# Kernel optimization log

Hardware: AMD Instinct MI355X
Metric: run time of the kernel (lower is better)

Reference implementation:

```python
import jax, jax.numpy as jnp
import numpy as np

N_AGENTS = 50000  # number of batch elements (agents); fixed num_segments
N_NEIGHBORS = 1600000  # total ragged neighbors flattened (avg degree 32)
STATE_DIM = 64
PHI_HID = 64
PHI_OUT = 64
RHO_HID = 64
ACT_DIM = 2


def setup_inputs() -> dict:
    key = jax.random.key(0)
    ks = jax.random.split(key, 6)
    s = lambda fan_in: 1.0 / np.sqrt(fan_in)
    neighbors = jax.random.normal(ks[0], (N_NEIGHBORS, STATE_DIM), dtype=jnp.float32)
    phi_w1 = jax.random.normal(ks[1], (STATE_DIM, PHI_HID), dtype=jnp.float32) * s(STATE_DIM)
    phi_b1 = jnp.zeros((PHI_HID,), dtype=jnp.float32)
    phi_w2 = jax.random.normal(ks[2], (PHI_HID, PHI_OUT), dtype=jnp.float32) * s(PHI_HID)
    phi_b2 = jnp.zeros((PHI_OUT,), dtype=jnp.float32)
    rho_w1 = jax.random.normal(ks[3], (PHI_OUT, RHO_HID), dtype=jnp.float32) * s(PHI_OUT)
    rho_b1 = jnp.zeros((RHO_HID,), dtype=jnp.float32)
    rho_w2 = jax.random.normal(ks[4], (RHO_HID, ACT_DIM), dtype=jnp.float32) * s(RHO_HID)
    rho_b2 = jnp.zeros((ACT_DIM,), dtype=jnp.float32)
    segment_ids = jnp.sort(jax.random.randint(ks[5], (N_NEIGHBORS,), 0, N_AGENTS, dtype=jnp.int32))
    return {
        "neighbors": neighbors,
        "phi_w1": phi_w1, "phi_b1": phi_b1, "phi_w2": phi_w2, "phi_b2": phi_b2,
        "rho_w1": rho_w1, "rho_b1": rho_b1, "rho_w2": rho_w2, "rho_b2": rho_b2,
        "segment_ids": segment_ids,
    }


def reference(neighbors, phi_w1, phi_b1, phi_w2, phi_b2,
              rho_w1, rho_b1, rho_w2, rho_b2, segment_ids):
    # phi MLP applied to every neighbor feature (vectorized over the flat ragged axis)
    h = jax.nn.relu(neighbors @ phi_w1 + phi_b1)          # [N_NEIGHBORS, PHI_HID]
    h = h @ phi_w2 + phi_b2                               # [N_NEIGHBORS, PHI_OUT]
    # per-agent sum over variable-length neighbor sets (the Python double loop in torch)
    summ = jax.ops.segment_sum(h, segment_ids, num_segments=N_AGENTS)  # [N_AGENTS, PHI_OUT]
    # rho MLP on pooled features
    r = jax.nn.relu(summ @ rho_w1 + rho_b1)               # [N_AGENTS, RHO_HID]
    return r @ rho_w2 + rho_b2                            # [N_AGENTS, ACT_DIM]
```

## Files before the change

kernel.cpp:

```cpp
#include <hip/hip_runtime.h>
#include <hip/hip_bf16.h>

#define N_AGENTS 50000
#define N_NEI    1600000
#define ROWS     128
#define PHI_BLOCKS (N_NEI / ROWS)

typedef __bf16 bf16_t;
typedef __attribute__((ext_vector_type(8))) __bf16 bf16x8;
typedef __attribute__((ext_vector_type(4))) __bf16 bf16x4;
typedef __attribute__((ext_vector_type(4))) float  f32x4;

#define SA 72
#define SO 66

__global__ __launch_bounds__(256) void phi_kernel(
    const float* __restrict__ nb,
    const float* __restrict__ w1g, const float* __restrict__ b1g,
    const float* __restrict__ w2g, const float* __restrict__ b2g,
    const int* __restrict__ seg, float* __restrict__ summ)
{
  __shared__ __align__(16) union {
    struct {
      bf16_t A[ROWS * SA];
      bf16_t Wt[2][64 * SA];
    } s;
    float outb[ROWS * SO];
  } u;
  __shared__ float biasf[2][64];
  __shared__ int sid[ROWS + 4];

  const int tid  = threadIdx.x;
  const int w    = tid >> 6;
  const int lane = tid & 63;
  const int m16  = lane & 15;
  const int q    = lane >> 4;
  const int base_row = blockIdx.x * ROWS;

  if (tid < ROWS) sid[tid] = seg[base_row + tid];
  if (tid < 64) biasf[0][tid] = b1g[tid];
  else if (tid < 128) biasf[1][tid - 64] = b2g[tid - 64];

  for (int i = tid; i < 4096; i += 256) {
    int k = i >> 6, n = i & 63;
    u.s.Wt[0][n * SA + k] = (bf16_t)w1g[i];
    u.s.Wt[1][n * SA + k] = (bf16_t)w2g[i];
  }

  {
    const float4* np4 = (const float4*)(nb + (size_t)base_row * 64);
    #pragma unroll
    for (int it = 0; it < 8; ++it) {
      int j = tid + it * 256;
      float4 v = np4[j];
      int row = j >> 4, col = (j & 15) * 4;
      bf16x4 p = { (bf16_t)v.x, (bf16_t)v.y, (bf16_t)v.z, (bf16_t)v.w };
      *(bf16x4*)&u.s.A[row * SA + col] = p;
    }
  }
  __syncthreads();

  const int rb = w * 32;
  bf16x8 bfr[4][2], afr[2][2];
  f32x4  acc[2][4];

  #pragma unroll
  for (int tn = 0; tn < 4; ++tn)
    #pragma unroll
    for (int kb = 0; kb < 2; ++kb)
      bfr[tn][kb] = *(const bf16x8*)&u.s.Wt[0][(tn * 16 + m16) * SA + kb * 32 + q * 8];
  #pragma unroll
  for (int tm = 0; tm < 2; ++tm)
    #pragma unroll
    for (int kb = 0; kb < 2; ++kb)
      afr[tm][kb] = *(const bf16x8*)&u.s.A[(rb + tm * 16 + m16) * SA + kb * 32 + q * 8];
  #pragma unroll
  for (int tm = 0; tm < 2; ++tm)
    #pragma unroll
    for (int tn = 0; tn < 4; ++tn) {
      f32x4 a = {0.f, 0.f, 0.f, 0.f};
      a = __builtin_amdgcn_mfma_f32_16x16x32_bf16(afr[tm][0], bfr[tn][0], a, 0, 0, 0);
      a = __builtin_amdgcn_mfma_f32_16x16x32_bf16(afr[tm][1], bfr[tn][1], a, 0, 0, 0);
      acc[tm][tn] = a;
    }
  #pragma unroll
  for (int tm = 0; tm < 2; ++tm)
    #pragma unroll
    for (int tn = 0; tn < 4; ++tn) {
      float bv = biasf[0][tn * 16 + m16];
      #pragma unroll
      for (int i = 0; i < 4; ++i) {
        float hv = fmaxf(acc[tm][tn][i] + bv, 0.f);
        u.s.A[(rb + tm * 16 + q * 4 + i) * SA + tn * 16 + m16] = (bf16_t)hv;
      }
    }

  #pragma unroll
  for (int tn = 0; tn < 4; ++tn)
    #pragma unroll
    for (int kb = 0; kb < 2; ++kb)
      bfr[tn][kb] = *(const bf16x8*)&u.s.Wt[1][(tn * 16 + m16) * SA + kb * 32 + q * 8];
  #pragma unroll
  for (int tm = 0; tm < 2; ++tm)
    #pragma unroll
    for (int kb = 0; kb < 2; ++kb)
      afr[tm][kb] = *(const bf16x8*)&u.s.A[(rb + tm * 16 + m16) * SA + kb * 32 + q * 8];
  __syncthreads();

  #pragma unroll
  for (int tm = 0; tm < 2; ++tm)
    #pragma unroll
    for (int tn = 0; tn < 4; ++tn) {
      f32x4 a = {0.f, 0.f, 0.f, 0.f};
      a = __builtin_amdgcn_mfma_f32_16x16x32_bf16(afr[tm][0], bfr[tn][0], a, 0, 0, 0);
      a = __builtin_amdgcn_mfma_f32_16x16x32_bf16(afr[tm][1], bfr[tn][1], a, 0, 0, 0);
      acc[tm][tn] = a;
    }
  #pragma unroll
  for (int tm = 0; tm < 2; ++tm)
    #pragma unroll
    for (int tn = 0; tn < 4; ++tn) {
      float bv = biasf[1][tn * 16 + m16];
      #pragma unroll
      for (int i = 0; i < 4; ++i)
        u.outb[(rb + tm * 16 + q * 4 + i) * SO + tn * 16 + m16] = acc[tm][tn][i] + bv;
    }

  float racc = 0.f;
  for (int r = rb; r < rb + 32; ++r) {
    racc += u.outb[r * SO + lane];
    int sr = sid[r];
    if (r == rb + 31 || sid[r + 1] != sr) {
      atomicAdd(summ + (size_t)sr * 64 + lane, racc);
      racc = 0.f;
    }
  }
}

__global__ __launch_bounds__(256) void rho_kernel(
    const float* __restrict__ summ,
    const float* __restrict__ w1g, const float* __restrict__ b1g,
    const float* __restrict__ w2g, const float* __restrict__ b2g,
    float* __restrict__ out)
{
  __shared__ float sw1[64 * 64];
  __shared__ float sw2[128];
  __shared__ float sb1[64];
  __shared__ float sb2[2];
  const int tid = threadIdx.x;
  for (int i = tid; i < 4096; i += 256) sw1[i] = w1g[i];
  if (tid < 128) sw2[tid] = w2g[tid];
  if (tid < 64)  sb1[tid] = b1g[tid];
  if (tid < 2)   sb2[tid] = b2g[tid];
  __syncthreads();

  int a = blockIdx.x * 256 + tid;
  if (a >= N_AGENTS) return;

  float x[64];
  const float4* xr = (const float4*)(summ + (size_t)a * 64);
  #pragma unroll
  for (int i = 0; i < 16; ++i) {
    float4 v = xr[i];
    x[4*i] = v.x; x[4*i+1] = v.y; x[4*i+2] = v.z; x[4*i+3] = v.w;
  }

  float o0 = sb2[0], o1 = sb2[1];
  for (int n = 0; n < 64; ++n) {
    float a0 = sb1[n], a1 = 0.f, a2 = 0.f, a3 = 0.f;
    #pragma unroll
    for (int k = 0; k < 64; k += 4) {
      a0 = fmaf(x[k],     sw1[(k)     * 64 + n], a0);
      a1 = fmaf(x[k + 1], sw1[(k + 1) * 64 + n], a1);
      a2 = fmaf(x[k + 2], sw1[(k + 2) * 64 + n], a2);
      a3 = fmaf(x[k + 3], sw1[(k + 3) * 64 + n], a3);
    }
    float h = fmaxf((a0 + a1) + (a2 + a3), 0.f);
    o0 = fmaf(h, sw2[2 * n],     o0);
    o1 = fmaf(h, sw2[2 * n + 1], o1);
  }
  *(float2*)(out + (size_t)a * 2) = make_float2(o0, o1);
}

extern "C" void kernel_launch(void* const* d_in, const int* in_sizes, int n_in,
                              void* d_out, int out_size, void* d_ws, size_t ws_size,
                              hipStream_t stream) {
  const float* neighbors = (const float*)d_in[0];
  const float* phi_w1    = (const float*)d_in[1];
  const float* phi_b1    = (const float*)d_in[2];
  const float* phi_w2    = (const float*)d_in[3];
  const float* phi_b2    = (const float*)d_in[4];
  const float* rho_w1    = (const float*)d_in[5];
  const float* rho_b1    = (const float*)d_in[6];
  const float* rho_w2    = (const float*)d_in[7];
  const float* rho_b2    = (const float*)d_in[8];
  const int*   seg       = (const int*)d_in[9];
  float* out  = (float*)d_out;
  float* summ = (float*)d_ws;

  hipMemsetAsync(summ, 0, (size_t)N_AGENTS * 64 * sizeof(float), stream);
  phi_kernel<<<PHI_BLOCKS, 256, 0, stream>>>(neighbors, phi_w1, phi_b1,
                                             phi_w2, phi_b2, seg, summ);
  rho_kernel<<<(N_AGENTS + 255) / 256, 256, 0, stream>>>(summ, rho_w1, rho_b1,
                                                         rho_w2, rho_b2, out);
}
```

Baseline: 606.9 us.

## Fold phi second layer into rho via linearity of segment sum

Because the second phi layer is linear, the segment sum of ReLU hidden activations is taken directly, and phi_w2 is folded into rho_w1 (Wc = W2·Rw1, bias scaled by per-agent neighbor count) in a small prep kernel. This removes the second per-neighbor MFMA GEMM and its LDS round trip. Weights are also prepacked once into MFMA fragment order and loaded with global_load_lds, and neighbor rows are written straight into fragment layout. It adds a count atomic per segment run and a tiny prep launch, and changes float summation order.

```diff
diff --git a/kernel.cpp b/kernel.cpp
--- a/kernel.cpp
+++ b/kernel.cpp
@@ -8,72 +8,108 @@
 
 typedef __bf16 bf16_t;
 typedef __attribute__((ext_vector_type(8))) __bf16 bf16x8;
-typedef __attribute__((ext_vector_type(4))) __bf16 bf16x4;
 typedef __attribute__((ext_vector_type(4))) float  f32x4;
 
-#define SA 72
 #define SO 66
 
-__global__ __launch_bounds__(256) void phi_kernel(
-    const float* __restrict__ nb,
-    const float* __restrict__ w1g, const float* __restrict__ b1g,
-    const float* __restrict__ w2g, const float* __restrict__ b2g,
-    const int* __restrict__ seg, float* __restrict__ summ)
+#define WS_SUMM   0
+#define WS_CNT    3200000
+#define WS_WC     3250000
+#define WS_BC     3254096
+#define WS_W1PK   3254160
+#define WS_ZERO_F 3250000
+
+__global__ __launch_bounds__(256) void prep_kernel(
+    const float* __restrict__ w1g, const float* __restrict__ w2g,
+    const float* __restrict__ b2g, const float* __restrict__ rw1g,
+    unsigned short* __restrict__ w1pack, float* __restrict__ Wc,
+    float* __restrict__ bc)
+{
+  const int tid = threadIdx.x;
+  if (blockIdx.x == 0) {
+    for (int i = tid; i < 4096; i += 256) {
+      int k = i >> 6, n = i & 63;
+      int tn = n >> 4, kb = k >> 5;
+      int l  = (n & 15) + 16 * ((k >> 3) & 3);
+      int j  = k & 7;
+      bf16_t bv = (bf16_t)w1g[i];
+      w1pack[((tn * 2 + kb) * 64 + l) * 8 + j] = *(unsigned short*)&bv;
+    }
+  } else {
+    for (int i = tid; i < 4096; i += 256) {
+      int h = i >> 6, n = i & 63;
+      float s = 0.f;
+      #pragma unroll 8
+      for (int o = 0; o < 64; ++o) s = fmaf(w2g[h * 64 + o], rw1g[o * 64 + n], s);
+      Wc[i] = s;
+    }
+    if (tid < 64) {
+      float s = 0.f;
+      for (int o = 0; o < 64; ++o) s = fmaf(b2g[o], rw1g[o * 64 + tid], s);
+      bc[tid] = s;
+    }
+  }
+}
+
+__global__ __launch_bounds__(256, 4) void phi_kernel(
+    const float* __restrict__ nb, const float* __restrict__ b1g,
+    const int* __restrict__ seg, const unsigned short* __restrict__ w1pack,
+    float* __restrict__ summH1, float* __restrict__ cnt)
 {
   __shared__ __align__(16) union {
     struct {
-      bf16_t A[ROWS * SA];
-      bf16_t Wt[2][64 * SA];
+      bf16_t Afr[16 * 64 * 8];
+      bf16_t Wfr[8 * 64 * 8];
     } s;
     float outb[ROWS * SO];
   } u;
-  __shared__ float biasf[2][64];
-  __shared__ int sid[ROWS + 4];
+  __shared__ float biasf[64];
+  __shared__ int sid[ROWS];
 
   const int tid  = threadIdx.x;
   const int w    = tid >> 6;
   const int lane = tid & 63;
   const int m16  = lane & 15;
   const int q    = lane >> 4;
-  const int base_row = blockIdx.x * ROWS;
-
-  if (tid < ROWS) sid[tid] = seg[base_row + tid];
-  if (tid < 64) biasf[0][tid] = b1g[tid];
-  else if (tid < 128) biasf[1][tid - 64] = b2g[tid - 64];
-
-  for (int i = tid; i < 4096; i += 256) {
-    int k = i >> 6, n = i & 63;
-    u.s.Wt[0][n * SA + k] = (bf16_t)w1g[i];
-    u.s.Wt[1][n * SA + k] = (bf16_t)w2g[i];
-  }
-
-  {
-    const float4* np4 = (const float4*)(nb + (size_t)base_row * 64);
-    #pragma unroll
-    for (int it = 0; it < 8; ++it) {
-      int j = tid + it * 256;
-      float4 v = np4[j];
-      int row = j >> 4, col = (j & 15) * 4;
-      bf16x4 p = { (bf16_t)v.x, (bf16_t)v.y, (bf16_t)v.z, (bf16_t)v.w };
-      *(bf16x4*)&u.s.A[row * SA + col] = p;
-    }
+  const long base = (long)blockIdx.x * ROWS;
+
+  if (tid < ROWS) sid[tid] = seg[base + tid];
+  if (tid < 64)  biasf[tid] = b1g[tid];
+
+  #pragma unroll
+  for (int c = 0; c < 2; ++c) {
+    int chunk = w * 2 + c;
+    __builtin_amdgcn_global_load_lds(
+        (const __attribute__((address_space(1))) void*)(w1pack + chunk * 512 + lane * 8),
+        (__attribute__((address_space(3))) void*)(&u.s.Wfr[chunk * 512]),
+        16, 0, 0);
+  }
+
+  #pragma unroll
+  for (int it = 0; it < 4; ++it) {
+    int tile = 2 * w + (it >> 1), kb = it & 1;
+    int row = tile * 16 + m16;
+    const float4* g = (const float4*)(nb + (base + row) * 64 + kb * 32 + q * 8);
+    float4 v0 = g[0], v1 = g[1];
+    bf16x8 p = { (bf16_t)v0.x, (bf16_t)v0.y, (bf16_t)v0.z, (bf16_t)v0.w,
+                 (bf16_t)v1.x, (bf16_t)v1.y, (bf16_t)v1.z, (bf16_t)v1.w };
+    *(bf16x8*)&u.s.Afr[((tile * 2 + kb) * 64 + lane) * 8] = p;
   }
   __syncthreads();
 
-  const int rb = w * 32;
-  bf16x8 bfr[4][2], afr[2][2];
-  f32x4  acc[2][4];
-
+  bf16x8 afr[2][2], bfr[4][2];
+  #pragma unroll
+  for (int tm = 0; tm < 2; ++tm)
+    #pragma unroll
+    for (int kb = 0; kb < 2; ++kb)
+      afr[tm][kb] = *(const bf16x8*)&u.s.Afr[(((2 * w + tm) * 2 + kb) * 64 + lane) * 8];
   #pragma unroll
   for (int tn = 0; tn < 4; ++tn)
     #pragma unroll
     for (int kb = 0; kb < 2; ++kb)
-      bfr[tn][kb] = *(const bf16x8*)&u.s.Wt[0][(tn * 16 + m16) * SA + kb * 32 + q * 8];
-  #pragma unroll
-  for (int tm = 0; tm < 2; ++tm)
-    #pragma unroll
-    for (int kb = 0; kb < 2; ++kb)
-      afr[tm][kb] = *(const bf16x8*)&u.s.A[(rb + tm * 16 + m16) * SA + kb * 32 + q * 8];
+      bfr[tn][kb] = *(const bf16x8*)&u.s.Wfr[((tn * 2 + kb) * 64 + lane) * 8];
+
+  f32x4 acc[2][4];
   #pragma unroll
   for (int tm = 0; tm < 2; ++tm)
     #pragma unroll
@@ -83,103 +119,77 @@
       a = __builtin_amdgcn_mfma_f32_16x16x32_bf16(afr[tm][1], bfr[tn][1], a, 0, 0, 0);
       acc[tm][tn] = a;
     }
+  __syncthreads();
+
+  const int rb = w * 32;
   #pragma unroll
   for (int tm = 0; tm < 2; ++tm)
     #pragma unroll
     for (int tn = 0; tn < 4; ++tn) {
-      float bv = biasf[0][tn * 16 + m16];
-      #pragma unroll
-      for (int i = 0; i < 4; ++i) {
-        float hv = fmaxf(acc[tm][tn][i] + bv, 0.f);
-        u.s.A[(rb + tm * 16 + q * 4 + i) * SA + tn * 16 + m16] = (bf16_t)hv;
-      }
-    }
-
-  #pragma unroll
-  for (int tn = 0; tn < 4; ++tn)
-    #pragma unroll
-    for (int kb = 0; kb < 2; ++kb)
-      bfr[tn][kb] = *(const bf16x8*)&u.s.Wt[1][(tn * 16 + m16) * SA + kb * 32 + q * 8];
-  #pragma unroll
-  for (int tm = 0; tm < 2; ++tm)
-    #pragma unroll
-    for (int kb = 0; kb < 2; ++kb)
-      afr[tm][kb] = *(const bf16x8*)&u.s.A[(rb + tm * 16 + m16) * SA + kb * 32 + q * 8];
-  __syncthreads();
-
-  #pragma unroll
-  for (int tm = 0; tm < 2; ++tm)
-    #pragma unroll
-    for (int tn = 0; tn < 4; ++tn) {
-      f32x4 a = {0.f, 0.f, 0.f, 0.f};
-      a = __builtin_amdgcn_mfma_f32_16x16x32_bf16(afr[tm][0], bfr[tn][0], a, 0, 0, 0);
-      a = __builtin_amdgcn_mfma_f32_16x16x32_bf16(afr[tm][1], bfr[tn][1], a, 0, 0, 0);
-      acc[tm][tn] = a;
-    }
-  #pragma unroll
-  for (int tm = 0; tm < 2; ++tm)
-    #pragma unroll
-    for (int tn = 0; tn < 4; ++tn) {
-      float bv = biasf[1][tn * 16 + m16];
+      float bv = biasf[tn * 16 + m16];
       #pragma unroll
       for (int i = 0; i < 4; ++i)
-        u.outb[(rb + tm * 16 + q * 4 + i) * SO + tn * 16 + m16] = acc[tm][tn][i] + bv;
+        u.outb[(rb + tm * 16 + q * 4 + i) * SO + tn * 16 + m16] =
+            fmaxf(acc[tm][tn][i] + bv, 0.f);
     }
 
   float racc = 0.f;
+  int runlen = 0;
   for (int r = rb; r < rb + 32; ++r) {
     racc += u.outb[r * SO + lane];
+    ++runlen;
     int sr = sid[r];
     if (r == rb + 31 || sid[r + 1] != sr) {
-      atomicAdd(summ + (size_t)sr * 64 + lane, racc);
+      atomicAdd(summH1 + (long)sr * 64 + lane, racc);
+      if (lane == 0) atomicAdd(cnt + sr, (float)runlen);
       racc = 0.f;
+      runlen = 0;
     }
   }
 }
 
 __global__ __launch_bounds__(256) void rho_kernel(
-    const float* __restrict__ summ,
-    const float* __restrict__ w1g, const float* __restrict__ b1g,
-    const float* __restrict__ w2g, const float* __restrict__ b2g,
-    float* __restrict__ out)
+    const float* __restrict__ summH1, const float* __restrict__ cnt,
+    const float* __restrict__ Wc, const float* __restrict__ bc,
+    const float* __restrict__ rb1g, const float* __restrict__ rw2g,
+    const float* __restrict__ rb2g, float* __restrict__ out)
 {
-  __shared__ float sw1[64 * 64];
-  __shared__ float sw2[128];
-  __shared__ float sb1[64];
-  __shared__ float sb2[2];
+  __shared__ float sW[64 * 64];
+  __shared__ float sbc[64], sb1[64], sw2[128], sb2[2];
   const int tid = threadIdx.x;
-  for (int i = tid; i < 4096; i += 256) sw1[i] = w1g[i];
-  if (tid < 128) sw2[tid] = w2g[tid];
-  if (tid < 64)  sb1[tid] = b1g[tid];
-  if (tid < 2)   sb2[tid] = b2g[tid];
+  for (int i = tid; i < 4096; i += 256) sW[i] = Wc[i];
+  if (tid < 64)  { sbc[tid] = bc[tid]; sb1[tid] = rb1g[tid]; }
+  if (tid < 128) sw2[tid] = rw2g[tid];
+  if (tid < 2)   sb2[tid] = rb2g[tid];
   __syncthreads();
 
   int a = blockIdx.x * 256 + tid;
   if (a >= N_AGENTS) return;
 
   float x[64];
-  const float4* xr = (const float4*)(summ + (size_t)a * 64);
+  const float4* xr = (const float4*)(summH1 + (long)a * 64);
   #pragma unroll
   for (int i = 0; i < 16; ++i) {
     float4 v = xr[i];
-    x[4*i] = v.x; x[4*i+1] = v.y; x[4*i+2] = v.z; x[4*i+3] = v.w;
-  }
+    x[4 * i] = v.x; x[4 * i + 1] = v.y; x[4 * i + 2] = v.z; x[4 * i + 3] = v.w;
+  }
+  float c = cnt[a];
 
   float o0 = sb2[0], o1 = sb2[1];
   for (int n = 0; n < 64; ++n) {
-    float a0 = sb1[n], a1 = 0.f, a2 = 0.f, a3 = 0.f;
+    float a0 = fmaf(c, sbc[n], sb1[n]), a1 = 0.f, a2 = 0.f, a3 = 0.f;
     #pragma unroll
     for (int k = 0; k < 64; k += 4) {
-      a0 = fmaf(x[k],     sw1[(k)     * 64 + n], a0);
-      a1 = fmaf(x[k + 1], sw1[(k + 1) * 64 + n], a1);
-      a2 = fmaf(x[k + 2], sw1[(k + 2) * 64 + n], a2);
-      a3 = fmaf(x[k + 3], sw1[(k + 3) * 64 + n], a3);
+      a0 = fmaf(x[k],     sW[(k)     * 64 + n], a0);
+      a1 = fmaf(x[k + 1], sW[(k + 1) * 64 + n], a1);
+      a2 = fmaf(x[k + 2], sW[(k + 2) * 64 + n], a2);
+      a3 = fmaf(x[k + 3], sW[(k + 3) * 64 + n], a3);
     }
     float h = fmaxf((a0 + a1) + (a2 + a3), 0.f);
     o0 = fmaf(h, sw2[2 * n],     o0);
     o1 = fmaf(h, sw2[2 * n + 1], o1);
   }
-  *(float2*)(out + (size_t)a * 2) = make_float2(o0, o1);
+  *(float2*)(out + (long)a * 2) = make_float2(o0, o1);
 }
 
 extern "C" void kernel_launch(void* const* d_in, const int* in_sizes, int n_in,
@@ -195,12 +205,20 @@
   const float* rho_w2    = (const float*)d_in[7];
   const float* rho_b2    = (const float*)d_in[8];
   const int*   seg       = (const int*)d_in[9];
-  float* out  = (float*)d_out;
-  float* summ = (float*)d_ws;
-
-  hipMemsetAsync(summ, 0, (size_t)N_AGENTS * 64 * sizeof(float), stream);
-  phi_kernel<<<PHI_BLOCKS, 256, 0, stream>>>(neighbors, phi_w1, phi_b1,
-                                             phi_w2, phi_b2, seg, summ);
-  rho_kernel<<<(N_AGENTS + 255) / 256, 256, 0, stream>>>(summ, rho_w1, rho_b1,
-                                                         rho_w2, rho_b2, out);
-}
+  float* out = (float*)d_out;
+
+  float* ws     = (float*)d_ws;
+  float* summH1 = ws + WS_SUMM;
+  float* cntp   = ws + WS_CNT;
+  float* Wc     = ws + WS_WC;
+  float* bc     = ws + WS_BC;
+  unsigned short* w1pack = (unsigned short*)(ws + WS_W1PK);
+
+  hipMemsetAsync(ws, 0, (size_t)WS_ZERO_F * sizeof(float), stream);
+  prep_kernel<<<2, 256, 0, stream>>>(phi_w1, phi_w2, phi_b2, rho_w1,
+                                     w1pack, Wc, bc);
+  phi_kernel<<<PHI_BLOCKS, 256, 0, stream>>>(neighbors, phi_b1, seg, w1pack,
+                                             summH1, cntp);
+  rho_kernel<<<(N_AGENTS + 255) / 256, 256, 0, stream>>>(summH1, cntp, Wc, bc,
+                                                         rho_b1, rho_w2, rho_b2, out);
+}
```

New measurement: 628.9 us. 1.04x slower.
